# Kernel tuning notes

Measured on AMD Instinct MI355X. Metric: run time of the kernel, lower is better.

Reference implementation:

```python
import jax, jax.numpy as jnp
import numpy as np

TEMPERATURE = 1.0
NEG = -1e9
EPS = 1e-8


def setup_inputs() -> dict:
    key = jax.random.key(0)
    k1, k2, k3 = jax.random.split(key, 3)
    B, H = 524288, 32
    scores = jax.random.normal(k1, (B, H), dtype=jnp.float32)
    rankings = jax.random.randint(k2, (B, H), 0, 33, dtype=jnp.int32)
    mask = jax.random.randint(k3, (B, H), 0, 2, dtype=jnp.int32).astype(bool)
    return {"scores": scores, "rankings": rankings, "mask": mask}


def reference(scores, rankings, mask):
    B, H = scores.shape
    # effective validity: horse present AND has a ranking > 0 (top_k=None)
    m = mask & (rankings > 0)
    # masked, temperature-scaled scores; -1e9 entries underflow to exactly 0 in softmax
    s = jnp.where(m, scores / TEMPERATURE, NEG)
    p = jax.nn.softmax(s, axis=1)  # [B, H], ~0 at invalid slots

    n_valid = jnp.sum(m, axis=1)  # [B]
    # ideal order: valid horses sorted by ranking ascending (invalid pushed to end)
    rank_key = jnp.where(m, rankings, jnp.iinfo(jnp.int32).max)
    rank_order = jnp.argsort(rank_key, axis=1)          # stable sort
    # prediction order: valid horses in original index order (matches torch.where)
    pos_order = jnp.argsort(~m, axis=1)                 # stable: valid first

    q = jnp.take_along_axis(p, rank_order, axis=1)      # ideal_probs, aligned by list position
    pr = jnp.take_along_axis(p, pos_order, axis=1)      # pred_probs,  aligned by list position

    # positions >= n_valid are padding
    valid_pos = jnp.arange(H)[None, :] < n_valid[:, None]
    q_safe = jnp.where(valid_pos, q, 1.0)
    pr_safe = jnp.where(valid_pos, pr, 1.0)
    # KL(ideal || pred) with the original's log(pred + 1e-8)
    kl_terms = q_safe * (jnp.log(q_safe) - jnp.log(pr_safe + EPS))
    kl = jnp.sum(jnp.where(valid_pos, kl_terms, 0.0), axis=1)  # [B]

    # rows with <= 1 valid ranked horse are skipped entirely
    row_ok = n_valid > 1
    n_rows = jnp.maximum(jnp.sum(row_ok), 1)
    return jnp.sum(jnp.where(row_ok, kl, 0.0)) / n_rows  # reduction='mean'
```

## Files before the change

### kernel.cpp

```cpp
#include <hip/hip_runtime.h>
#include <stdint.h>


#define H 32
#define BLK 256
#define WPB 4

typedef unsigned short us2 __attribute__((ext_vector_type(2)));
union UP { uint32_t u; us2 v; };

template<int CTRL>
__device__ __forceinline__ uint32_t dppmov_u(uint32_t x) {
    return (uint32_t)__builtin_amdgcn_update_dpp(0, (int)x, CTRL, 0xF, 0xF, true);
}
template<int CTRL>
__device__ __forceinline__ float dppmov_f(float x) {
    return __int_as_float(
        __builtin_amdgcn_update_dpp(0, __float_as_int(x), CTRL, 0xF, 0xF, true));
}

__device__ __forceinline__ float half_sum32(float v) {
    v += dppmov_f<0x111>(v);
    v += dppmov_f<0x112>(v);
    v += dppmov_f<0x114>(v);
    v += dppmov_f<0x118>(v);
    v += dppmov_f<0x142>(v);
    return v;
}

__device__ __forceinline__ uint32_t cex(uint32_t W, uint32_t Wo, bool tm) {
    UP a, b, mn, mx;
    a.u = W; b.u = Wo;
    mn.v.x = a.v.x < b.v.x ? a.v.x : b.v.x;
    mx.v.x = a.v.x < b.v.x ? b.v.x : a.v.x;
    mn.v.y = a.v.y < b.v.y ? a.v.y : b.v.y;
    mx.v.y = a.v.y < b.v.y ? b.v.y : a.v.y;
    return tm ? mx.u : mn.u;
}

__global__ __launch_bounds__(BLK) void listwise_kernel(
    const float* __restrict__ scores,
    const int* __restrict__ rankings,
    const unsigned char* __restrict__ mask_u8,
    float* __restrict__ part_kl,
    float* __restrict__ part_cnt,
    int nrows, int ipw)
{
    __shared__ float s_kl[WPB], s_cnt[WPB];

    const int tid  = threadIdx.x;
    const int lane = tid & 63;
    const int wid  = tid >> 6;
    const int e5   = lane & 31;
    const int h    = lane >> 5;
    const uint32_t e5u = (uint32_t)e5;

    const long long wave_g  = (long long)blockIdx.x * WPB + wid;
    const long long tgroups = ((long long)nrows + 3) >> 2;
    const long long gbeg = wave_g * ipw;
    const long long gend = (gbeg + ipw < tgroups) ? (gbeg + ipw) : tgroups;

    unsigned char probe = mask_u8[lane];
    const bool mask_is_i32 =
        (__ballot(((lane & 3) != 0) && (probe != 0)) == 0ull);

    float kl_acc = 0.0f, cnt_acc = 0.0f;

    if (gbeg < gend) {
        const size_t maxidx = (size_t)nrows * H - 1;

        size_t b0 = (size_t)gbeg * 128 + lane; if (b0 > maxidx) b0 = maxidx;
        size_t b1 = (size_t)gbeg * 128 + 64 + lane; if (b1 > maxidx) b1 = maxidx;
        int   rv0 = rankings[b0], rv1 = rankings[b1];
        float sv0 = scores[b0],   sv1 = scores[b1];
        uint32_t mm0, mm1;
        if (mask_is_i32) {
            mm0 = (uint32_t)((const int*)mask_u8)[b0];
            mm1 = (uint32_t)((const int*)mask_u8)[b1];
        } else {
            mm0 = (uint32_t)mask_u8[b0];
            mm1 = (uint32_t)mask_u8[b1];
        }

        for (long long g = gbeg; g < gend; ++g) {
            const long long gn = (g + 1 < gend) ? (g + 1) : g;
            size_t nb0 = (size_t)gn * 128 + lane; if (nb0 > maxidx) nb0 = maxidx;
            size_t nb1 = (size_t)gn * 128 + 64 + lane; if (nb1 > maxidx) nb1 = maxidx;
            const int   xrv0 = rankings[nb0], xrv1 = rankings[nb1];
            const float xsv0 = scores[nb0],   xsv1 = scores[nb1];
            uint32_t xmm0, xmm1;
            if (mask_is_i32) {
                xmm0 = (uint32_t)((const int*)mask_u8)[nb0];
                xmm1 = (uint32_t)((const int*)mask_u8)[nb1];
            } else {
                xmm0 = (uint32_t)mask_u8[nb0];
                xmm1 = (uint32_t)mask_u8[nb1];
            }

            const int rowA = (int)(4 * g) + h;
            const int rowB = rowA + 2;
            const bool vA = (rowA < nrows) && (mm0 != 0u) && (rv0 > 0);
            const bool vB = (rowB < nrows) && (mm1 != 0u) && (rv1 > 0);

            const float sA = __uint_as_float(((__float_as_uint(sv0) + 0x8000u) >> 16) << 16);
            const float sB = __uint_as_float(((__float_as_uint(sv1) + 0x8000u) >> 16) << 16);

            const uint32_t kA = vA ? (((uint32_t)rv0 << 5) | e5u) : (0x8000u | e5u);
            const uint32_t kB = vB ? (((uint32_t)rv1 << 5) | e5u) : (0x8000u | e5u);
            uint32_t W = kA | (kB << 16);

            const unsigned long long bmA = __ballot(vA);
            const unsigned long long bmB = __ballot(vB);
            const uint32_t lo_pcA = __builtin_popcount((uint32_t)bmA);
            const uint32_t lo_pcB = __builtin_popcount((uint32_t)bmB);
            const uint32_t belowA = __builtin_amdgcn_mbcnt_hi(
                (uint32_t)(bmA >> 32),
                __builtin_amdgcn_mbcnt_lo((uint32_t)bmA, 0u));
            const uint32_t belowB = __builtin_amdgcn_mbcnt_hi(
                (uint32_t)(bmB >> 32),
                __builtin_amdgcn_mbcnt_lo((uint32_t)bmB, 0u));
            const int qA = (int)belowA - (h ? (int)lo_pcA : 0);
            const int qB = (int)belowB - (h ? (int)lo_pcB : 0);
            const int nvA = h ? __builtin_popcount((uint32_t)(bmA >> 32)) : (int)lo_pcA;
            const int nvB = h ? __builtin_popcount((uint32_t)(bmB >> 32)) : (int)lo_pcB;
            const int slotA = (vA ? qA : nvA + (e5 - qA)) + (h << 5);
            const int slotB = (vB ? qB : nvB + (e5 - qB)) + (h << 5);
            const float gA = __int_as_float(
                __builtin_amdgcn_ds_permute(slotA << 2, __float_as_int(sA)));
            const float gB = __int_as_float(
                __builtin_amdgcn_ds_permute(slotB << 2, __float_as_int(sB)));

            #pragma unroll
            for (int k = 2; k <= 32; k <<= 1) {
                #pragma unroll
                for (int j = k >> 1; j > 0; j >>= 1) {
                    uint32_t Wo;
                    if (j == 1)      Wo = dppmov_u<0xB1>(W);
                    else if (j == 2) Wo = dppmov_u<0x4E>(W);
                    else             Wo = (uint32_t)__shfl_xor((int)W, j);
                    const bool tm = (((e5 & j) == 0) != ((e5 & k) == 0));
                    W = cex(W, Wo, tm);
                }
            }

            const uint32_t WA = W & 0xFFFFu, WB = W >> 16;
            const bool vA2 = (WA & 0x8000u) == 0u;
            const bool vB2 = (WB & 0x8000u) == 0u;
            const int iA = (int)(WA & 31u), iB = (int)(WB & 31u);
            const float srA = __int_as_float(__builtin_amdgcn_ds_bpermute(
                (((h << 5) | iA) << 2), __float_as_int(sA)));
            const float srB = __int_as_float(__builtin_amdgcn_ds_bpermute(
                (((h << 5) | iB) << 2), __float_as_int(sB)));

            float eA = __expf(srA); eA = vA2 ? eA : 0.0f;
            float eB = __expf(srB); eB = vB2 ? eB : 0.0f;
            const float tA = eA * (srA - gA);
            const float tB = eB * (srB - gB);

            const float seA = half_sum32(eA);
            const float seB = half_sum32(eB);
            const float nmA = half_sum32(tA);
            const float nmB = half_sum32(tB);

            const float cA = (nvA > 1) ? __fdividef(nmA, seA) : 0.0f;
            const float cB = (nvB > 1) ? __fdividef(nmB, seB) : 0.0f;
            const bool tip = (e5 == 31);
            kl_acc  += tip ? (cA + cB) : 0.0f;
            cnt_acc += tip ? ((nvA > 1 ? 1.0f : 0.0f) + (nvB > 1 ? 1.0f : 0.0f))
                           : 0.0f;

            rv0 = xrv0; rv1 = xrv1; sv0 = xsv0; sv1 = xsv1;
            mm0 = xmm0; mm1 = xmm1;
        }
    }

    #pragma unroll
    for (int m = 32; m >= 1; m >>= 1) {
        kl_acc  += __shfl_xor(kl_acc, m);
        cnt_acc += __shfl_xor(cnt_acc, m);
    }
    if (lane == 0) { s_kl[wid] = kl_acc; s_cnt[wid] = cnt_acc; }
    __syncthreads();
    if (tid == 0) {
        part_kl[blockIdx.x]  = s_kl[0] + s_kl[1] + s_kl[2] + s_kl[3];
        part_cnt[blockIdx.x] = s_cnt[0] + s_cnt[1] + s_cnt[2] + s_cnt[3];
    }
}

__global__ __launch_bounds__(256) void finalize_kernel(
    const float* __restrict__ part_kl,
    const float* __restrict__ part_cnt,
    float* __restrict__ out, int nblk)
{
    float k = 0.0f, c = 0.0f;
    for (int i = threadIdx.x; i < nblk; i += 256) {
        k += part_kl[i];
        c += part_cnt[i];
    }
    #pragma unroll
    for (int m = 32; m >= 1; m >>= 1) {
        k += __shfl_xor(k, m);
        c += __shfl_xor(c, m);
    }
    __shared__ float sk[4], sc[4];
    const int wid = threadIdx.x >> 6;
    if ((threadIdx.x & 63) == 0) { sk[wid] = k; sc[wid] = c; }
    __syncthreads();
    if (threadIdx.x == 0) {
        float K = sk[0] + sk[1] + sk[2] + sk[3];
        float C = sc[0] + sc[1] + sc[2] + sc[3];
        if (C < 1.0f) C = 1.0f;
        out[0] = K / C;
    }
}

extern "C" void kernel_launch(void* const* d_in, const int* in_sizes, int n_in,
                              void* d_out, int out_size, void* d_ws, size_t ws_size,
                              hipStream_t stream) {
    const float* scores = (const float*)d_in[0];
    const int* rankings = (const int*)d_in[1];
    const unsigned char* mask = (const unsigned char*)d_in[2];
    float* out = (float*)d_out;

    const int total = in_sizes[0];
    const int nrows = total / H;
    const int blocks = 2048;
    const long long tgroups = ((long long)nrows + 3) >> 2;
    const long long waves = (long long)blocks * WPB;
    int ipw = (int)((tgroups + waves - 1) / waves);
    if (ipw < 1) ipw = 1;

    float* part_kl  = (float*)d_ws;
    float* part_cnt = (float*)d_ws + blocks;

    listwise_kernel<<<blocks, BLK, 0, stream>>>(
        scores, rankings, mask, part_kl, part_cnt, nrows, ipw);

    finalize_kernel<<<1, 256, 0, stream>>>(part_kl, part_cnt, out, blocks);
}
```

Before: 206.9 us.

## Process two row-groups per iteration with deeper prefetch and precomputed sort masks

The main loop now handles two 4-row groups per iteration. It loads 256 elements per prefetch and takes a fast path that skips index clamping when the block is fully in bounds. The bitonic compare-exchange direction masks are precomputed once per lane into a register array and applied with bitwise selects. The packed 16-bit min/max now uses elementwise builtins, and the j=8 shuffle becomes a DPP row move. These changes aim to raise memory-level parallelism and cut per-step ALU work, at the cost of more registers (15 mask registers plus doubled prefetch buffers), which may reduce occupancy.

```diff
diff --git a/kernel.cpp b/kernel.cpp
--- a/kernel.cpp
+++ b/kernel.cpp
@@ -28,14 +28,128 @@
     return v;
 }
 
-__device__ __forceinline__ uint32_t cex(uint32_t W, uint32_t Wo, bool tm) {
-    UP a, b, mn, mx;
-    a.u = W; b.u = Wo;
-    mn.v.x = a.v.x < b.v.x ? a.v.x : b.v.x;
-    mx.v.x = a.v.x < b.v.x ? b.v.x : a.v.x;
-    mn.v.y = a.v.y < b.v.y ? a.v.y : b.v.y;
-    mx.v.y = a.v.y < b.v.y ? b.v.y : a.v.y;
-    return tm ? mx.u : mn.u;
+__device__ __forceinline__ void proc_group(
+    const uint32_t (&DM)[15],
+    int rvA, int rvB, float svA, float svB, uint32_t mmA, uint32_t mmB,
+    int rowA, int nrows, int e5, int h,
+    float& kl_acc, float& cnt_acc)
+{
+    const int rowB = rowA + 2;
+    const bool vA = (rowA < nrows) && (mmA != 0u) && (rvA > 0);
+    const bool vB = (rowB < nrows) && (mmB != 0u) && (rvB > 0);
+
+    const float sA = __uint_as_float(((__float_as_uint(svA) + 0x8000u) >> 16) << 16);
+    const float sB = __uint_as_float(((__float_as_uint(svB) + 0x8000u) >> 16) << 16);
+
+    const uint32_t e5u = (uint32_t)e5;
+    const uint32_t kA = vA ? (((uint32_t)rvA << 5) | e5u) : (0x8000u | e5u);
+    const uint32_t kB = vB ? (((uint32_t)rvB << 5) | e5u) : (0x8000u | e5u);
+    uint32_t W = kA | (kB << 16);
+
+    const unsigned long long bmA = __ballot(vA);
+    const unsigned long long bmB = __ballot(vB);
+    const uint32_t lo_pcA = __builtin_popcount((uint32_t)bmA);
+    const uint32_t lo_pcB = __builtin_popcount((uint32_t)bmB);
+    const uint32_t belowA = __builtin_amdgcn_mbcnt_hi(
+        (uint32_t)(bmA >> 32), __builtin_amdgcn_mbcnt_lo((uint32_t)bmA, 0u));
+    const uint32_t belowB = __builtin_amdgcn_mbcnt_hi(
+        (uint32_t)(bmB >> 32), __builtin_amdgcn_mbcnt_lo((uint32_t)bmB, 0u));
+    const int qA = (int)belowA - (h ? (int)lo_pcA : 0);
+    const int qB = (int)belowB - (h ? (int)lo_pcB : 0);
+    const int nvA = h ? __builtin_popcount((uint32_t)(bmA >> 32)) : (int)lo_pcA;
+    const int nvB = h ? __builtin_popcount((uint32_t)(bmB >> 32)) : (int)lo_pcB;
+    const int slotA = (vA ? qA : nvA + (e5 - qA)) + (h << 5);
+    const int slotB = (vB ? qB : nvB + (e5 - qB)) + (h << 5);
+    const float gA = __int_as_float(
+        __builtin_amdgcn_ds_permute(slotA << 2, __float_as_int(sA)));
+    const float gB = __int_as_float(
+        __builtin_amdgcn_ds_permute(slotB << 2, __float_as_int(sB)));
+
+    int sidx = 0;
+    #pragma unroll
+    for (int k = 2; k <= 32; k <<= 1) {
+        #pragma unroll
+        for (int j = k >> 1; j > 0; j >>= 1) {
+            uint32_t Wo;
+            if (j == 1)      Wo = dppmov_u<0xB1>(W);
+            else if (j == 2) Wo = dppmov_u<0x4E>(W);
+            else if (j == 8) Wo = dppmov_u<0x128>(W);
+            else             Wo = (uint32_t)__shfl_xor((int)W, j);
+            UP a, b, mn, mx;
+            a.u = W; b.u = Wo;
+            mn.v = __builtin_elementwise_min(a.v, b.v);
+            mx.v = __builtin_elementwise_max(a.v, b.v);
+            const uint32_t D = DM[sidx]; ++sidx;
+            W = (mn.u & ~D) | (mx.u & D);
+        }
+    }
+
+    const uint32_t WA = W & 0xFFFFu, WB = W >> 16;
+    const bool vA2 = (WA & 0x8000u) == 0u;
+    const bool vB2 = (WB & 0x8000u) == 0u;
+    const int iA = (int)(WA & 31u), iB = (int)(WB & 31u);
+    const float srA = __int_as_float(__builtin_amdgcn_ds_bpermute(
+        (((h << 5) | iA) << 2), __float_as_int(sA)));
+    const float srB = __int_as_float(__builtin_amdgcn_ds_bpermute(
+        (((h << 5) | iB) << 2), __float_as_int(sB)));
+
+    float eA = __expf(srA); eA = vA2 ? eA : 0.0f;
+    float eB = __expf(srB); eB = vB2 ? eB : 0.0f;
+    const float tA = eA * (srA - gA);
+    const float tB = eB * (srB - gB);
+
+    const float seA = half_sum32(eA);
+    const float seB = half_sum32(eB);
+    const float nmA = half_sum32(tA);
+    const float nmB = half_sum32(tB);
+
+    const float cA = (nvA > 1) ? __fdividef(nmA, seA) : 0.0f;
+    const float cB = (nvB > 1) ? __fdividef(nmB, seB) : 0.0f;
+    if (e5 == 31) {
+        kl_acc  += cA + cB;
+        cnt_acc += (nvA > 1 ? 1.0f : 0.0f) + (nvB > 1 ? 1.0f : 0.0f);
+    }
+}
+
+__device__ __forceinline__ void load_pair(
+    const float* __restrict__ scores, const int* __restrict__ rankings,
+    const unsigned char* __restrict__ mask_u8, bool mask_is_i32,
+    size_t base, int lane, size_t total,
+    int& r0, int& r1, int& r2, int& r3,
+    float& s0, float& s1, float& s2, float& s3,
+    uint32_t& m0, uint32_t& m1, uint32_t& m2, uint32_t& m3)
+{
+    if (base + 256 <= total) {
+        const size_t o = base + (size_t)lane;
+        r0 = rankings[o];       r1 = rankings[o + 64];
+        r2 = rankings[o + 128]; r3 = rankings[o + 192];
+        s0 = scores[o];         s1 = scores[o + 64];
+        s2 = scores[o + 128];   s3 = scores[o + 192];
+        if (mask_is_i32) {
+            const int* mp = (const int*)mask_u8;
+            m0 = (uint32_t)mp[o];       m1 = (uint32_t)mp[o + 64];
+            m2 = (uint32_t)mp[o + 128]; m3 = (uint32_t)mp[o + 192];
+        } else {
+            m0 = mask_u8[o];       m1 = mask_u8[o + 64];
+            m2 = mask_u8[o + 128]; m3 = mask_u8[o + 192];
+        }
+    } else {
+        const size_t mi = total - 1;
+        size_t o0 = base + (size_t)lane;        if (o0 > mi) o0 = mi;
+        size_t o1 = base + (size_t)lane + 64;   if (o1 > mi) o1 = mi;
+        size_t o2 = base + (size_t)lane + 128;  if (o2 > mi) o2 = mi;
+        size_t o3 = base + (size_t)lane + 192;  if (o3 > mi) o3 = mi;
+        r0 = rankings[o0]; r1 = rankings[o1]; r2 = rankings[o2]; r3 = rankings[o3];
+        s0 = scores[o0];   s1 = scores[o1];   s2 = scores[o2];   s3 = scores[o3];
+        if (mask_is_i32) {
+            const int* mp = (const int*)mask_u8;
+            m0 = (uint32_t)mp[o0]; m1 = (uint32_t)mp[o1];
+            m2 = (uint32_t)mp[o2]; m3 = (uint32_t)mp[o3];
+        } else {
+            m0 = mask_u8[o0]; m1 = mask_u8[o1];
+            m2 = mask_u8[o2]; m3 = mask_u8[o3];
+        }
+    }
 }
 
 __global__ __launch_bounds__(BLK) void listwise_kernel(
@@ -53,124 +167,63 @@
     const int wid  = tid >> 6;
     const int e5   = lane & 31;
     const int h    = lane >> 5;
-    const uint32_t e5u = (uint32_t)e5;
 
     const long long wave_g  = (long long)blockIdx.x * WPB + wid;
     const long long tgroups = ((long long)nrows + 3) >> 2;
     const long long gbeg = wave_g * ipw;
-    const long long gend = (gbeg + ipw < tgroups) ? (gbeg + ipw) : tgroups;
+    const long long gend0 = gbeg + ipw;
+    const long long gend = (gend0 < tgroups) ? gend0 : tgroups;
 
     unsigned char probe = mask_u8[lane];
     const bool mask_is_i32 =
         (__ballot(((lane & 3) != 0) && (probe != 0)) == 0ull);
 
+    uint32_t DM[15];
+    {
+        int s = 0;
+        #pragma unroll
+        for (int k = 2; k <= 32; k <<= 1)
+            #pragma unroll
+            for (int j = k >> 1; j > 0; j >>= 1)
+                DM[s++] = ((((e5 & j) == 0) != ((e5 & k) == 0))
+                               ? 0xFFFFFFFFu : 0u);
+    }
+
     float kl_acc = 0.0f, cnt_acc = 0.0f;
 
     if (gbeg < gend) {
-        const size_t maxidx = (size_t)nrows * H - 1;
-
-        size_t b0 = (size_t)gbeg * 128 + lane; if (b0 > maxidx) b0 = maxidx;
-        size_t b1 = (size_t)gbeg * 128 + 64 + lane; if (b1 > maxidx) b1 = maxidx;
-        int   rv0 = rankings[b0], rv1 = rankings[b1];
-        float sv0 = scores[b0],   sv1 = scores[b1];
-        uint32_t mm0, mm1;
-        if (mask_is_i32) {
-            mm0 = (uint32_t)((const int*)mask_u8)[b0];
-            mm1 = (uint32_t)((const int*)mask_u8)[b1];
-        } else {
-            mm0 = (uint32_t)mask_u8[b0];
-            mm1 = (uint32_t)mask_u8[b1];
-        }
-
-        for (long long g = gbeg; g < gend; ++g) {
-            const long long gn = (g + 1 < gend) ? (g + 1) : g;
-            size_t nb0 = (size_t)gn * 128 + lane; if (nb0 > maxidx) nb0 = maxidx;
-            size_t nb1 = (size_t)gn * 128 + 64 + lane; if (nb1 > maxidx) nb1 = maxidx;
-            const int   xrv0 = rankings[nb0], xrv1 = rankings[nb1];
-            const float xsv0 = scores[nb0],   xsv1 = scores[nb1];
-            uint32_t xmm0, xmm1;
-            if (mask_is_i32) {
-                xmm0 = (uint32_t)((const int*)mask_u8)[nb0];
-                xmm1 = (uint32_t)((const int*)mask_u8)[nb1];
-            } else {
-                xmm0 = (uint32_t)mask_u8[nb0];
-                xmm1 = (uint32_t)mask_u8[nb1];
-            }
-
-            const int rowA = (int)(4 * g) + h;
-            const int rowB = rowA + 2;
-            const bool vA = (rowA < nrows) && (mm0 != 0u) && (rv0 > 0);
-            const bool vB = (rowB < nrows) && (mm1 != 0u) && (rv1 > 0);
-
-            const float sA = __uint_as_float(((__float_as_uint(sv0) + 0x8000u) >> 16) << 16);
-            const float sB = __uint_as_float(((__float_as_uint(sv1) + 0x8000u) >> 16) << 16);
-
-            const uint32_t kA = vA ? (((uint32_t)rv0 << 5) | e5u) : (0x8000u | e5u);
-            const uint32_t kB = vB ? (((uint32_t)rv1 << 5) | e5u) : (0x8000u | e5u);
-            uint32_t W = kA | (kB << 16);
-
-            const unsigned long long bmA = __ballot(vA);
-            const unsigned long long bmB = __ballot(vB);
-            const uint32_t lo_pcA = __builtin_popcount((uint32_t)bmA);
-            const uint32_t lo_pcB = __builtin_popcount((uint32_t)bmB);
-            const uint32_t belowA = __builtin_amdgcn_mbcnt_hi(
-                (uint32_t)(bmA >> 32),
-                __builtin_amdgcn_mbcnt_lo((uint32_t)bmA, 0u));
-            const uint32_t belowB = __builtin_amdgcn_mbcnt_hi(
-                (uint32_t)(bmB >> 32),
-                __builtin_amdgcn_mbcnt_lo((uint32_t)bmB, 0u));
-            const int qA = (int)belowA - (h ? (int)lo_pcA : 0);
-            const int qB = (int)belowB - (h ? (int)lo_pcB : 0);
-            const int nvA = h ? __builtin_popcount((uint32_t)(bmA >> 32)) : (int)lo_pcA;
-            const int nvB = h ? __builtin_popcount((uint32_t)(bmB >> 32)) : (int)lo_pcB;
-            const int slotA = (vA ? qA : nvA + (e5 - qA)) + (h << 5);
-            const int slotB = (vB ? qB : nvB + (e5 - qB)) + (h << 5);
-            const float gA = __int_as_float(
-                __builtin_amdgcn_ds_permute(slotA << 2, __float_as_int(sA)));
-            const float gB = __int_as_float(
-                __builtin_amdgcn_ds_permute(slotB << 2, __float_as_int(sB)));
-
-            #pragma unroll
-            for (int k = 2; k <= 32; k <<= 1) {
-                #pragma unroll
-                for (int j = k >> 1; j > 0; j >>= 1) {
-                    uint32_t Wo;
-                    if (j == 1)      Wo = dppmov_u<0xB1>(W);
-                    else if (j == 2) Wo = dppmov_u<0x4E>(W);
-                    else             Wo = (uint32_t)__shfl_xor((int)W, j);
-                    const bool tm = (((e5 & j) == 0) != ((e5 & k) == 0));
-                    W = cex(W, Wo, tm);
-                }
-            }
-
-            const uint32_t WA = W & 0xFFFFu, WB = W >> 16;
-            const bool vA2 = (WA & 0x8000u) == 0u;
-            const bool vB2 = (WB & 0x8000u) == 0u;
-            const int iA = (int)(WA & 31u), iB = (int)(WB & 31u);
-            const float srA = __int_as_float(__builtin_amdgcn_ds_bpermute(
-                (((h << 5) | iA) << 2), __float_as_int(sA)));
-            const float srB = __int_as_float(__builtin_amdgcn_ds_bpermute(
-                (((h << 5) | iB) << 2), __float_as_int(sB)));
-
-            float eA = __expf(srA); eA = vA2 ? eA : 0.0f;
-            float eB = __expf(srB); eB = vB2 ? eB : 0.0f;
-            const float tA = eA * (srA - gA);
-            const float tB = eB * (srB - gB);
-
-            const float seA = half_sum32(eA);
-            const float seB = half_sum32(eB);
-            const float nmA = half_sum32(tA);
-            const float nmB = half_sum32(tB);
-
-            const float cA = (nvA > 1) ? __fdividef(nmA, seA) : 0.0f;
-            const float cB = (nvB > 1) ? __fdividef(nmB, seB) : 0.0f;
-            const bool tip = (e5 == 31);
-            kl_acc  += tip ? (cA + cB) : 0.0f;
-            cnt_acc += tip ? ((nvA > 1 ? 1.0f : 0.0f) + (nvB > 1 ? 1.0f : 0.0f))
-                           : 0.0f;
-
-            rv0 = xrv0; rv1 = xrv1; sv0 = xsv0; sv1 = xsv1;
-            mm0 = xmm0; mm1 = xmm1;
+        const size_t total = (size_t)nrows * H;
+        const long long npairs = (gend - gbeg + 1) >> 1;
+
+        size_t base = (size_t)gbeg * 128;
+        int      cr0, cr1, cr2, cr3;
+        float    cs0, cs1, cs2, cs3;
+        uint32_t cm0, cm1, cm2, cm3;
+        load_pair(scores, rankings, mask_u8, mask_is_i32, base, lane, total,
+                  cr0, cr1, cr2, cr3, cs0, cs1, cs2, cs3, cm0, cm1, cm2, cm3);
+
+        for (long long t = 0; t < npairs; ++t) {
+            const long long G = gbeg + 2 * t;
+
+            const bool last = (t + 1 >= npairs);
+            const size_t nbase = last ? base : (base + 256);
+            int      xr0, xr1, xr2, xr3;
+            float    xs0, xs1, xs2, xs3;
+            uint32_t xm0, xm1, xm2, xm3;
+            load_pair(scores, rankings, mask_u8, mask_is_i32, nbase, lane, total,
+                      xr0, xr1, xr2, xr3, xs0, xs1, xs2, xs3,
+                      xm0, xm1, xm2, xm3);
+
+            proc_group(DM, cr0, cr1, cs0, cs1, cm0, cm1,
+                       (int)(4 * G) + h, nrows, e5, h, kl_acc, cnt_acc);
+            const int rowA1 = (G + 1 < gend) ? (int)(4 * (G + 1)) + h : nrows;
+            proc_group(DM, cr2, cr3, cs2, cs3, cm2, cm3,
+                       rowA1, nrows, e5, h, kl_acc, cnt_acc);
+
+            cr0 = xr0; cr1 = xr1; cr2 = xr2; cr3 = xr3;
+            cs0 = xs0; cs1 = xs1; cs2 = xs2; cs3 = xs3;
+            cm0 = xm0; cm1 = xm1; cm2 = xm2; cm3 = xm3;
+            base = nbase;
         }
     }
 
```

Measured after the change: 209.6 us. About the same (+1.3%).
